# Performance work log

Hardware: AMD Instinct MI355X
Metric: run time of the kernel (lower is better)

## Reference

```python
import jax, jax.numpy as jnp
import numpy as np

N_MIN = 16
N_TABLES = 16
PER_LEVEL_SCALE = 1.3195079565048218
MAX_TABLE = 2 ** 19
H1, H2, H3 = 1, 2654435761, 805459861
OFFS = np.array([[0,0,0],[0,0,1],[0,1,0],[0,1,1],[1,0,0],[1,0,1],[1,1,0],[1,1,1]], dtype=np.int32)

def _levels():
    N_l, sizes, max_direct = [], [], 0
    for i in range(N_TABLES):
        res = int(np.ceil(N_MIN * np.exp(i * np.log(PER_LEVEL_SCALE)) - 1.0)) + 1
        ts = res ** 3
        ts = ts if ts % 8 == 0 else ((ts + 7) // 8) * 8
        ts = min(MAX_TABLE, ts)
        if ts == res ** 3:
            max_direct = i
        N_l.append(res); sizes.append(ts)
    return N_l, sizes, max_direct

N_L, SIZES, MAX_DIRECT = _levels()

def hash_encode(pos, grids):
    # pos: [N,3] in [0,1); grids: [16, MAX_TABLE, 2] (levels padded to MAX_TABLE)
    feats = []
    for l in range(N_TABLES):
        uvz = pos * jnp.float32(N_L[l])
        iuv_f = jnp.floor(uvz)
        f = uvz - iuv_f                                   # fractional part [N,3]
        corners = iuv_f.astype(jnp.int32)[:, None, :] + OFFS[None]  # [N,8,3]
        if l <= MAX_DIRECT:
            R = N_L[l]
            idx = (corners[..., 2] * (R * R) + corners[..., 1] * R + corners[..., 0]) % SIZES[l]
        else:
            cu = corners.astype(jnp.uint32)
            h = (cu[..., 0] * jnp.uint32(H1)) ^ (cu[..., 1] * jnp.uint32(H2)) ^ (cu[..., 2] * jnp.uint32(H3))
            idx = (h % jnp.uint32(SIZES[l])).astype(jnp.int32)
        c = grids[l][idx]                                 # gather -> [N,8,2]
        fx, fy, fz = f[:, 0:1], f[:, 1:2], f[:, 2:3]
        c00 = c[:, 0] * (1 - fx) + c[:, 4] * fx
        c01 = c[:, 1] * (1 - fx) + c[:, 5] * fx
        c10 = c[:, 2] * (1 - fx) + c[:, 6] * fx
        c11 = c[:, 3] * (1 - fx) + c[:, 7] * fx
        c0 = c00 * (1 - fy) + c10 * fy
        c1 = c01 * (1 - fy) + c11 * fy
        feats.append(c0 * (1 - fz) + c1 * fy)  # NOTE: c1*fy (not fz) replicates source exactly
    return jnp.concatenate(feats, axis=-1)  # [N, 32]

def setup_inputs():
    key = jax.random.key(0)
    ks = jax.random.split(key, 7)
    N = 1048576  # max_samples(512) * batch_size(2048)
    x = jax.random.uniform(ks[0], (N, 19), dtype=jnp.float32)  # pos(3) in [0,1) + dir feats(16)
    grids = (jax.random.uniform(ks[1], (N_TABLES, MAX_TABLE, 2), dtype=jnp.float32) * 2.0 - 1.0) * 1e-4
    h = 64
    w_sigma1 = jax.random.normal(ks[2], (32, h), dtype=jnp.float32) / np.sqrt(32).astype(np.float32)
    w_sigma2 = jax.random.normal(ks[3], (h, 16), dtype=jnp.float32) / np.sqrt(h).astype(np.float32)
    w_c1 = jax.random.normal(ks[4], (32, h), dtype=jnp.float32) / np.sqrt(32).astype(np.float32)
    w_c2 = jax.random.normal(ks[5], (h, h), dtype=jnp.float32) / np.sqrt(h).astype(np.float32)
    w_c3 = jax.random.normal(ks[6], (h, 3), dtype=jnp.float32) / np.sqrt(h).astype(np.float32)
    return {"x": x, "grids": grids, "w_sigma1": w_sigma1, "w_sigma2": w_sigma2,
            "w_c1": w_c1, "w_c2": w_c2, "w_c3": w_c3}

def reference(x, grids, w_sigma1, w_sigma2, w_c1, w_c2, w_c3):
    pos, direc = x[:, :3], x[:, 3:]
    enc = hash_encode(pos, grids)                       # [N,32]
    out = jax.nn.relu(enc @ w_sigma1) @ w_sigma2        # [N,16]
    sigma = out[:, 0]
    ci = jnp.concatenate([direc, out], axis=-1)         # [N,32]
    color = jax.nn.sigmoid(jax.nn.relu(jax.nn.relu(ci @ w_c1) @ w_c2) @ w_c3)  # [N,3]
    return jnp.concatenate([color, sigma[:, None]], axis=-1)  # [N,4]
```

## Files before the change

kernel.cpp:

```cpp
#include <hip/hip_runtime.h>
#include <math.h>


#define BLOCK 256
#define NTAB  (16*524288)
#define PITCH 88

constexpr int      kNL[16] = {16,22,28,37,49,65,85,112,148,195,257,338,446,589,777,1025};
constexpr unsigned kSZ[16] = {4096u,10648u,21952u,50656u,117656u,274632u,
                              524288u,524288u,524288u,524288u,524288u,
                              524288u,524288u,524288u,524288u,524288u};

typedef __attribute__((ext_vector_type(8))) short short8;
typedef __attribute__((ext_vector_type(4))) float float4v;

__device__ __forceinline__ short f2bf(float f) {
    unsigned u = __float_as_uint(f);
    unsigned r = u + 0x7fffu + ((u >> 16) & 1u);
    return (short)(r >> 16);
}
__device__ __forceinline__ float bf2f(short h) {
    return __uint_as_float(((unsigned)(unsigned short)h) << 16);
}
__device__ __forceinline__ unsigned pk2(float a, float b) {
    return ((unsigned)(unsigned short)f2bf(b) << 16) | (unsigned)(unsigned short)f2bf(a);
}
__device__ __forceinline__ float pe0(unsigned u) { return __uint_as_float(u << 16); }
__device__ __forceinline__ float pe1(unsigned u) { return __uint_as_float(u & 0xffff0000u); }

__device__ __forceinline__ unsigned trilerp_pack(const unsigned* vv, float fx, float fy, float fz)
{
    const float w0x = 1.f-fx, w0y = 1.f-fy, w0z = 1.f-fz;
    float e0, e1;
    {
        float c00 = pe0(vv[0])*w0x + pe0(vv[4])*fx;
        float c01 = pe0(vv[1])*w0x + pe0(vv[5])*fx;
        float c10 = pe0(vv[2])*w0x + pe0(vv[6])*fx;
        float c11 = pe0(vv[3])*w0x + pe0(vv[7])*fx;
        float c0 = c00*w0y + c10*fy;
        float c1 = c01*w0y + c11*fy;
        e0 = c0*w0z + c1*fy;
    }
    {
        float c00 = pe1(vv[0])*w0x + pe1(vv[4])*fx;
        float c01 = pe1(vv[1])*w0x + pe1(vv[5])*fx;
        float c10 = pe1(vv[2])*w0x + pe1(vv[6])*fx;
        float c11 = pe1(vv[3])*w0x + pe1(vv[7])*fx;
        float c0 = c00*w0y + c10*fy;
        float c1 = c01*w0y + c11*fy;
        e1 = c0*w0z + c1*fy;
    }
    return pk2(e0, e1);
}

__global__ void pack_pos(const float* __restrict__ x, float4* __restrict__ pos4, int n)
{
    int i = blockIdx.x * BLOCK + threadIdx.x;
    if (i >= n) return;
    const float* xr = x + (size_t)i * 19;
    pos4[i] = make_float4(xr[0], xr[1], xr[2], 0.f);
}

__global__ void conv_tables(const float* __restrict__ grids, unsigned* __restrict__ tbu)
{
    int i = blockIdx.x * BLOCK + threadIdx.x;
    if (i >= NTAB) return;
    float2 v = ((const float2*)grids)[i];
    tbu[i] = pk2(v.x, v.y);
}

__global__ void pack_wfrag(const float* __restrict__ w1, const float* __restrict__ w2,
                           const float* __restrict__ wc1, const float* __restrict__ wc2,
                           const float* __restrict__ wc3, uint4* __restrict__ wf)
{
    int lane = threadIdx.x;
    if (lane >= 64) return;
    int cn = lane & 15, q = lane >> 4;

    auto pack8 = [](const float* src, int stride) -> uint4 {
        uint4 r;
        r.x = pk2(src[0*stride], src[1*stride]);
        r.y = pk2(src[2*stride], src[3*stride]);
        r.z = pk2(src[4*stride], src[5*stride]);
        r.w = pk2(src[6*stride], src[7*stride]);
        return r;
    };

    int f = 0;
    for (int nt = 0; nt < 4; ++nt)
        wf[(f++)*64 + lane] = pack8(w1 + (q*8)*64 + nt*16 + cn, 64);
    for (int c = 0; c < 2; ++c)
        wf[(f++)*64 + lane] = pack8(w2 + (c*32 + q*8)*16 + cn, 16);
    for (int nt = 0; nt < 4; ++nt)
        wf[(f++)*64 + lane] = pack8(wc1 + (q*8)*64 + nt*16 + cn, 64);
    for (int c = 0; c < 2; ++c)
        for (int nt = 0; nt < 4; ++nt)
            wf[(f++)*64 + lane] = pack8(wc2 + (c*32 + q*8)*64 + nt*16 + cn, 64);
    for (int c = 0; c < 2; ++c) {
        if (cn < 3) wf[(f++)*64 + lane] = pack8(wc3 + (c*32 + q*8)*3 + cn, 3);
        else { uint4 z; z.x = z.y = z.z = z.w = 0u; wf[(f++)*64 + lane] = z; }
    }
}

template<int L>
__device__ __forceinline__ void gather4(const float4* __restrict__ pos4,
                                        const unsigned* __restrict__ tball,
                                        unsigned* __restrict__ encu,
                                        int n, int p0, int cnt)
{
    constexpr int R = kNL[L];
    constexpr unsigned S = kSZ[L];
    constexpr unsigned H2c = 2654435761u, H3c = 805459861u;
    const unsigned* __restrict__ tbu = tball + (size_t)L * 524288u;

    unsigned vv[4][8];
    float fxa[4], fya[4], fza[4];
    #pragma unroll
    for (int q = 0; q < 4; ++q) {
        if (q >= cnt) continue;
        float4 p = pos4[p0+q];
        const float Rf = (float)R;
        float ux = p.x*Rf, uy = p.y*Rf, uz = p.z*Rf;
        float gx = floorf(ux), gy = floorf(uy), gz = floorf(uz);
        fxa[q] = ux-gx; fya[q] = uy-gy; fza[q] = uz-gz;
        int ix = (int)gx, iy = (int)gy, iz = (int)gz;

        unsigned tc[4];
        #pragma unroll
        for (int c = 0; c < 4; ++c) {
            int yb = c >> 1, zb = c & 1;
            tc[c] = (unsigned)(iy+yb)*H2c ^ (unsigned)(iz+zb)*H3c;
        }
        if ((ix & 1) == 0) {
            #pragma unroll
            for (int c = 0; c < 4; ++c) {
                unsigned idx0 = ((unsigned)ix ^ tc[c]) & (S-1u);
                uint2 pr = *(const uint2*)(tbu + (idx0 & ~1u));
                unsigned swp = idx0 & 1u;
                vv[q][c]   = swp ? pr.y : pr.x;
                vv[q][4+c] = swp ? pr.x : pr.y;
            }
        } else {
            #pragma unroll
            for (int c = 0; c < 4; ++c) {
                unsigned idx0 = ((unsigned)ix     ^ tc[c]) & (S-1u);
                unsigned idx1 = ((unsigned)(ix+1) ^ tc[c]) & (S-1u);
                vv[q][c]   = tbu[idx0];
                vv[q][4+c] = tbu[idx1];
            }
        }
    }

    unsigned pkd[4];
    #pragma unroll
    for (int q = 0; q < 4; ++q) {
        if (q >= cnt) continue;
        pkd[q] = trilerp_pack(vv[q], fxa[q], fya[q], fza[q]);
    }

    unsigned* d = encu + (size_t)L*n + p0;
    if (cnt == 4) {
        uint4 o; o.x = pkd[0]; o.y = pkd[1]; o.z = pkd[2]; o.w = pkd[3];
        *(uint4*)d = o;
    } else {
        for (int q = 0; q < cnt; ++q) d[q] = pkd[q];
    }
}

__global__ __launch_bounds__(BLOCK)
void enc_all(const float4* __restrict__ pos4, const unsigned* __restrict__ tball,
             unsigned* __restrict__ encu, int n, int byA)
{
    const int bx = blockIdx.x;
    const int by = blockIdx.y;

    if (by < byA) {
        int p0 = (by*BLOCK + threadIdx.x) * 4;
        if (p0 >= n) return;
        int cnt = min(4, n - p0);
        switch (bx) {
            case 0: gather4< 6>(pos4,tball,encu,n,p0,cnt); break;
            case 1: gather4< 7>(pos4,tball,encu,n,p0,cnt); break;
            case 2: gather4< 8>(pos4,tball,encu,n,p0,cnt); break;
            case 3: gather4< 9>(pos4,tball,encu,n,p0,cnt); break;
            case 4: gather4<10>(pos4,tball,encu,n,p0,cnt); break;
            case 5: gather4<11>(pos4,tball,encu,n,p0,cnt); break;
            case 6: gather4<12>(pos4,tball,encu,n,p0,cnt); break;
            case 7: gather4<13>(pos4,tball,encu,n,p0,cnt); break;
        }
    } else {
        int q4 = (n + 3) / 4;
        int quarter = bx & 3;
        int jb = quarter * q4;
        int je = min(n, jb + q4);
        int p0 = jb + ((by-byA)*BLOCK + threadIdx.x) * 4;
        if (p0 >= je) return;
        int cnt = min(4, je - p0);
        if (bx < 4) gather4<14>(pos4,tball,encu,n,p0,cnt);
        else        gather4<15>(pos4,tball,encu,n,p0,cnt);
    }
}

template<int LV>
__device__ __forceinline__ void enc_addr(float4 p, const unsigned* __restrict__ tball,
                                         unsigned vv[8], float& fx, float& fy, float& fz)
{
    constexpr int R = kNL[LV];
    constexpr unsigned S = kSZ[LV];
    constexpr unsigned H2c = 2654435761u, H3c = 805459861u;
    const unsigned* __restrict__ tb = tball + (size_t)LV * 524288u;
    const float Rf = (float)R;
    float ux = p.x*Rf, uy = p.y*Rf, uz = p.z*Rf;
    float gx = floorf(ux), gy = floorf(uy), gz = floorf(uz);
    fx = ux-gx; fy = uy-gy; fz = uz-gz;
    int ix = (int)gx, iy = (int)gy, iz = (int)gz;

    if (LV >= 3) {
        unsigned tc[4];
        #pragma unroll
        for (int c = 0; c < 4; ++c) {
            int yb = c >> 1, zb = c & 1;
            tc[c] = (unsigned)(iy+yb)*H2c ^ (unsigned)(iz+zb)*H3c;
        }
        if ((ix & 1) == 0) {
            #pragma unroll
            for (int c = 0; c < 4; ++c) {
                unsigned h0 = (unsigned)ix ^ tc[c];
                unsigned base = (h0 & ~1u) % S;
                uint2 pr = *(const uint2*)(tb + base);
                unsigned swp = h0 & 1u;
                vv[c]   = swp ? pr.y : pr.x;
                vv[4+c] = swp ? pr.x : pr.y;
            }
        } else {
            #pragma unroll
            for (int c = 0; c < 4; ++c) {
                vv[c]   = tb[(((unsigned)ix)     ^ tc[c]) % S];
                vv[4+c] = tb[(((unsigned)(ix+1)) ^ tc[c]) % S];
            }
        }
    } else {
        #pragma unroll
        for (int j = 0; j < 8; ++j) {
            int ox = ix + ((j>>2)&1);
            int oy = iy + ((j>>1)&1);
            int oz = iz + (j&1);
            vv[j] = tb[(unsigned)((oz*(R*R) + oy*R + ox) % (int)S)];
        }
    }
}

__device__ __forceinline__ short8 ldfrag(const uint4* __restrict__ wf, int f, int lane) {
    union { uint4 u; short8 s; } cv;
    cv.u = wf[f*64 + lane];
    return cv.s;
}

__global__ __launch_bounds__(BLOCK)
void mlp_mfma(const float* __restrict__ x,
              const float4* __restrict__ pos4,
              const unsigned* __restrict__ tbu,
              const unsigned* __restrict__ encu,
              const uint4* __restrict__ wf,
              float* __restrict__ out, int n)
{
    __shared__ unsigned short s_scr[4][2][16*PITCH];
    __shared__ float s_sig[4][16];
    __shared__ float s_col[4][16][4];
    __shared__ float s_dir[4][304];
    __shared__ unsigned s_low[4][6][16];

    const int t = threadIdx.x;
    const int lane = t & 63;
    const int wave = t >> 6;
    const int m = lane & 15;
    const int q = lane >> 4;
    const int cn = m;
    const int blk = blockIdx.x * 64;
    const int pt  = blk + wave*16 + m;
    const int ptc = pt < n ? pt : n - 1;
    const int p0w = blk + wave*16;

    const float4v zero = {0.f, 0.f, 0.f, 0.f};

    {
        int npts = n - p0w; if (npts > 16) npts = 16; if (npts < 0) npts = 0;
        int nfl = npts * 19;
        const float* xs = x + (size_t)p0w * 19;
        float* sd = s_dir[wave];
        #pragma unroll
        for (int it = 0; it < 5; ++it) {
            int idx = it*64 + lane;
            if (idx < nfl) sd[idx] = xs[idx];
        }
    }

    {
        int lv = lane >> 4, pm = lane & 15;
        int pp = p0w + pm; if (pp >= n) pp = n - 1;
        float4 p = pos4[pp];
        unsigned vv[8]; float fx, fy, fz;
        switch (lv) {
            case 0: enc_addr<0>(p, tbu, vv, fx, fy, fz); break;
            case 1: enc_addr<1>(p, tbu, vv, fx, fy, fz); break;
            case 2: enc_addr<2>(p, tbu, vv, fx, fy, fz); break;
            default: enc_addr<3>(p, tbu, vv, fx, fy, fz); break;
        }
        s_low[wave][lv][pm] = trilerp_pack(vv, fx, fy, fz);
    }
    if (lane < 32) {
        int lv = 4 + (lane >> 4), pm = lane & 15;
        int pp = p0w + pm; if (pp >= n) pp = n - 1;
        float4 p = pos4[pp];
        unsigned vv[8]; float fx, fy, fz;
        if (lv == 4) enc_addr<4>(p, tbu, vv, fx, fy, fz);
        else         enc_addr<5>(p, tbu, vv, fx, fy, fz);
        s_low[wave][lv][pm] = trilerp_pack(vv, fx, fy, fz);
    }

    union { unsigned u[4]; short8 s; } a1;
    #pragma unroll
    for (int i = 0; i < 4; ++i) {
        int lv = q*4 + i;
        if (lv < 6) a1.u[i] = s_low[wave][lv][m];
        else        a1.u[i] = encu[(size_t)lv*n + ptc];
    }

    short8 bw1[4], bw2[2], bwc1[4];
    #pragma unroll
    for (int nt = 0; nt < 4; ++nt) bw1[nt] = ldfrag(wf, nt, lane);
    #pragma unroll
    for (int c = 0; c < 2; ++c)    bw2[c]  = ldfrag(wf, 4 + c, lane);
    #pragma unroll
    for (int nt = 0; nt < 4; ++nt) bwc1[nt] = ldfrag(wf, 6 + nt, lane);

    float4v h[4];
    #pragma unroll
    for (int nt = 0; nt < 4; ++nt) {
        h[nt] = __builtin_amdgcn_mfma_f32_16x16x32_bf16(a1.s, bw1[nt], zero, 0, 0, 0);
        #pragma unroll
        for (int r = 0; r < 4; ++r) h[nt][r] = fmaxf(h[nt][r], 0.f);
    }

    unsigned short* sA = &s_scr[wave][0][0];
    unsigned short* sB = &s_scr[wave][1][0];
    #pragma unroll
    for (int nt = 0; nt < 4; ++nt)
        #pragma unroll
        for (int r = 0; r < 4; ++r)
            sA[(q*4+r)*PITCH + nt*16 + cn] = (unsigned short)f2bf(h[nt][r]);
    short8 ah[2];
    #pragma unroll
    for (int c = 0; c < 2; ++c)
        ah[c] = *(const short8*)&sA[m*PITCH + c*32 + q*8];

    float4v o = __builtin_amdgcn_mfma_f32_16x16x32_bf16(ah[0], bw2[0], zero, 0, 0, 0);
    o = __builtin_amdgcn_mfma_f32_16x16x32_bf16(ah[1], bw2[1], o, 0, 0, 0);
    if (cn == 0) {
        #pragma unroll
        for (int r = 0; r < 4; ++r) s_sig[wave][q*4+r] = o[r];
    }

    #pragma unroll
    for (int r = 0; r < 4; ++r)
        sB[(q*4+r)*PITCH + cn] = (unsigned short)f2bf(o[r]);
    short8 ov = *(const short8*)&sB[m*PITCH + (q >= 2 ? (q-2)*8 : 0)];

    union { unsigned u[4]; short8 s; } ci_hi, ci_lo;
    if (q < 2) {
        const float* sd = s_dir[wave];
        int rm = ptc - p0w; if (rm < 0) rm = 0;
        #pragma unroll
        for (int i = 0; i < 4; ++i) {
            float d0 = sd[rm*19 + 3 + q*8 + 2*i];
            float d1 = sd[rm*19 + 3 + q*8 + 2*i + 1];
            short h0 = f2bf(d0), h1 = f2bf(d1);
            ci_hi.u[i] = ((unsigned)(unsigned short)h1 << 16) | (unsigned)(unsigned short)h0;
            short l0 = f2bf(d0 - bf2f(h0)), l1 = f2bf(d1 - bf2f(h1));
            ci_lo.u[i] = ((unsigned)(unsigned short)l1 << 16) | (unsigned)(unsigned short)l0;
        }
    } else {
        ci_hi.s = ov;
        #pragma unroll
        for (int i = 0; i < 4; ++i) ci_lo.u[i] = 0u;
    }

    float4v hc[4];
    #pragma unroll
    for (int nt = 0; nt < 4; ++nt) {
        hc[nt] = __builtin_amdgcn_mfma_f32_16x16x32_bf16(ci_hi.s, bwc1[nt], zero, 0, 0, 0);
        hc[nt] = __builtin_amdgcn_mfma_f32_16x16x32_bf16(ci_lo.s, bwc1[nt], hc[nt], 0, 0, 0);
        #pragma unroll
        for (int r = 0; r < 4; ++r) hc[nt][r] = fmaxf(hc[nt][r], 0.f);
    }

    short8 bwc2[2][4], bwc3[2];
    #pragma unroll
    for (int c = 0; c < 2; ++c)
        #pragma unroll
        for (int nt = 0; nt < 4; ++nt)
            bwc2[c][nt] = ldfrag(wf, 10 + c*4 + nt, lane);
    #pragma unroll
    for (int c = 0; c < 2; ++c) bwc3[c] = ldfrag(wf, 18 + c, lane);

    #pragma unroll
    for (int nt = 0; nt < 4; ++nt)
        #pragma unroll
        for (int r = 0; r < 4; ++r) {
            float v = hc[nt][r];
            short hi = f2bf(v);
            sA[(q*4+r)*PITCH + nt*16 + cn] = (unsigned short)hi;
            sB[(q*4+r)*PITCH + nt*16 + cn] = (unsigned short)f2bf(v - bf2f(hi));
        }
    short8 ghi[2], glo[2];
    #pragma unroll
    for (int c = 0; c < 2; ++c) {
        ghi[c] = *(const short8*)&sA[m*PITCH + c*32 + q*8];
        glo[c] = *(const short8*)&sB[m*PITCH + c*32 + q*8];
    }

    float4v g[4];
    #pragma unroll
    for (int nt = 0; nt < 4; ++nt) {
        float4v acc = __builtin_amdgcn_mfma_f32_16x16x32_bf16(ghi[0], bwc2[0][nt], zero, 0, 0, 0);
        acc = __builtin_amdgcn_mfma_f32_16x16x32_bf16(glo[0], bwc2[0][nt], acc, 0, 0, 0);
        acc = __builtin_amdgcn_mfma_f32_16x16x32_bf16(ghi[1], bwc2[1][nt], acc, 0, 0, 0);
        acc = __builtin_amdgcn_mfma_f32_16x16x32_bf16(glo[1], bwc2[1][nt], acc, 0, 0, 0);
        #pragma unroll
        for (int r = 0; r < 4; ++r) acc[r] = fmaxf(acc[r], 0.f);
        g[nt] = acc;
    }

    #pragma unroll
    for (int nt = 0; nt < 4; ++nt)
        #pragma unroll
        for (int r = 0; r < 4; ++r) {
            float v = g[nt][r];
            short hi = f2bf(v);
            sA[(q*4+r)*PITCH + nt*16 + cn] = (unsigned short)hi;
            sB[(q*4+r)*PITCH + nt*16 + cn] = (unsigned short)f2bf(v - bf2f(hi));
        }
    short8 uhi[2], ulo[2];
    #pragma unroll
    for (int c = 0; c < 2; ++c) {
        uhi[c] = *(const short8*)&sA[m*PITCH + c*32 + q*8];
        ulo[c] = *(const short8*)&sB[m*PITCH + c*32 + q*8];
    }

    float4v col = __builtin_amdgcn_mfma_f32_16x16x32_bf16(uhi[0], bwc3[0], zero, 0, 0, 0);
    col = __builtin_amdgcn_mfma_f32_16x16x32_bf16(ulo[0], bwc3[0], col, 0, 0, 0);
    col = __builtin_amdgcn_mfma_f32_16x16x32_bf16(uhi[1], bwc3[1], col, 0, 0, 0);
    col = __builtin_amdgcn_mfma_f32_16x16x32_bf16(ulo[1], bwc3[1], col, 0, 0, 0);
    #pragma unroll
    for (int r = 0; r < 4; ++r)
        col[r] = 1.f / (1.f + __expf(-col[r]));

    if (cn < 3) {
        #pragma unroll
        for (int r = 0; r < 4; ++r) s_col[wave][q*4+r][cn] = col[r];
    }

    __builtin_amdgcn_s_waitcnt(0);
    int pfi = lane >> 2, c4 = lane & 3;
    int pout = blk + wave*16 + pfi;
    if (pout < n) {
        float v = (c4 == 3) ? s_sig[wave][pfi] : s_col[wave][pfi][c4];
        out[(size_t)pout*4 + c4] = v;
    }
}

extern "C" void kernel_launch(void* const* d_in, const int* in_sizes, int n_in,
                              void* d_out, int out_size, void* d_ws, size_t ws_size,
                              hipStream_t stream) {
    const float* x     = (const float*)d_in[0];
    const float* grids = (const float*)d_in[1];
    const float* w1    = (const float*)d_in[2];
    const float* w2    = (const float*)d_in[3];
    const float* wc1   = (const float*)d_in[4];
    const float* wc2   = (const float*)d_in[5];
    const float* wc3   = (const float*)d_in[6];
    float* out = (float*)d_out;

    int n = in_sizes[0] / 19;
    size_t encB = (size_t)16 * n * sizeof(unsigned);
    size_t posB = (size_t)n * sizeof(float4);
    size_t tabB = (size_t)NTAB * sizeof(unsigned);

    char* p = (char*)d_ws;
    unsigned* encu = (unsigned*)p;
    float4*   pos4 = (float4*)(p + encB);
    unsigned* tbu  = (unsigned*)(p + encB + posB);
    uint4*    wf   = (uint4*)(p + encB + posB + tabB);

    pack_pos<<<(n + BLOCK - 1) / BLOCK, BLOCK, 0, stream>>>(x, pos4, n);
    conv_tables<<<(NTAB + BLOCK - 1) / BLOCK, BLOCK, 0, stream>>>(grids, tbu);
    pack_wfrag<<<1, 64, 0, stream>>>(w1, w2, wc1, wc2, wc3, wf);

    int byA = (n + BLOCK*4 - 1) / (BLOCK*4);
    int q4  = (n + 3) / 4;
    int byB = (q4 + BLOCK*4 - 1) / (BLOCK*4);
    dim3 ge(8, byA + byB);
    enc_all<<<ge, BLOCK, 0, stream>>>(pos4, tbu, encu, n, byA);

    mlp_mfma<<<(n + 63) / 64, BLOCK, 0, stream>>>(x, pos4, tbu, encu, wf, out, n);
}
```

Measured before the change: 554.3 us.

## Merge prep kernels into one launch and spread low-level encoding across waves

Combines the three preprocessing kernels (position packing, table bf16 conversion, weight fragment packing) into a single launch with block-range dispatch, removing two kernel launches and their gaps. In the MLP kernel, each wave now computes one low-resolution level for all 64 points of the block, so the level choice no longer diverges within a wave. The results are shared through block-level LDS, which requires a new __syncthreads. The encu loads for the high levels are hoisted to the top of the kernel so their latency overlaps with the low-level gathers.

```diff
diff --git a/kernel.cpp b/kernel.cpp
--- a/kernel.cpp
+++ b/kernel.cpp
@@ -53,52 +53,54 @@
     return pk2(e0, e1);
 }
 
-__global__ void pack_pos(const float* __restrict__ x, float4* __restrict__ pos4, int n)
+__global__ __launch_bounds__(BLOCK)
+void prep_all(const float* __restrict__ x, const float* __restrict__ grids,
+              const float* __restrict__ w1, const float* __restrict__ w2,
+              const float* __restrict__ wc1, const float* __restrict__ wc2,
+              const float* __restrict__ wc3,
+              float4* __restrict__ pos4, unsigned* __restrict__ tbu,
+              uint4* __restrict__ wf, int n, int nTabBlk, int nPosBlk)
 {
-    int i = blockIdx.x * BLOCK + threadIdx.x;
-    if (i >= n) return;
-    const float* xr = x + (size_t)i * 19;
-    pos4[i] = make_float4(xr[0], xr[1], xr[2], 0.f);
-}
-
-__global__ void conv_tables(const float* __restrict__ grids, unsigned* __restrict__ tbu)
-{
-    int i = blockIdx.x * BLOCK + threadIdx.x;
-    if (i >= NTAB) return;
-    float2 v = ((const float2*)grids)[i];
-    tbu[i] = pk2(v.x, v.y);
-}
-
-__global__ void pack_wfrag(const float* __restrict__ w1, const float* __restrict__ w2,
-                           const float* __restrict__ wc1, const float* __restrict__ wc2,
-                           const float* __restrict__ wc3, uint4* __restrict__ wf)
-{
-    int lane = threadIdx.x;
-    if (lane >= 64) return;
-    int cn = lane & 15, q = lane >> 4;
-
-    auto pack8 = [](const float* src, int stride) -> uint4 {
-        uint4 r;
-        r.x = pk2(src[0*stride], src[1*stride]);
-        r.y = pk2(src[2*stride], src[3*stride]);
-        r.z = pk2(src[4*stride], src[5*stride]);
-        r.w = pk2(src[6*stride], src[7*stride]);
-        return r;
-    };
-
-    int f = 0;
-    for (int nt = 0; nt < 4; ++nt)
-        wf[(f++)*64 + lane] = pack8(w1 + (q*8)*64 + nt*16 + cn, 64);
-    for (int c = 0; c < 2; ++c)
-        wf[(f++)*64 + lane] = pack8(w2 + (c*32 + q*8)*16 + cn, 16);
-    for (int nt = 0; nt < 4; ++nt)
-        wf[(f++)*64 + lane] = pack8(wc1 + (q*8)*64 + nt*16 + cn, 64);
-    for (int c = 0; c < 2; ++c)
-        for (int nt = 0; nt < 4; ++nt)
-            wf[(f++)*64 + lane] = pack8(wc2 + (c*32 + q*8)*64 + nt*16 + cn, 64);
-    for (int c = 0; c < 2; ++c) {
-        if (cn < 3) wf[(f++)*64 + lane] = pack8(wc3 + (c*32 + q*8)*3 + cn, 3);
-        else { uint4 z; z.x = z.y = z.z = z.w = 0u; wf[(f++)*64 + lane] = z; }
+    const int b = blockIdx.x;
+    if (b < nTabBlk) {
+        int i = b * BLOCK + threadIdx.x;
+        if (i < NTAB) {
+            float2 v = ((const float2*)grids)[i];
+            tbu[i] = pk2(v.x, v.y);
+        }
+    } else if (b < nTabBlk + nPosBlk) {
+        int i = (b - nTabBlk) * BLOCK + threadIdx.x;
+        if (i < n) {
+            const float* xr = x + (size_t)i * 19;
+            pos4[i] = make_float4(xr[0], xr[1], xr[2], 0.f);
+        }
+    } else {
+        int lane = threadIdx.x;
+        if (lane < 64) {
+            int cn = lane & 15, q = lane >> 4;
+            auto pack8 = [](const float* src, int stride) -> uint4 {
+                uint4 r;
+                r.x = pk2(src[0*stride], src[1*stride]);
+                r.y = pk2(src[2*stride], src[3*stride]);
+                r.z = pk2(src[4*stride], src[5*stride]);
+                r.w = pk2(src[6*stride], src[7*stride]);
+                return r;
+            };
+            int f = 0;
+            for (int nt = 0; nt < 4; ++nt)
+                wf[(f++)*64 + lane] = pack8(w1 + (q*8)*64 + nt*16 + cn, 64);
+            for (int c = 0; c < 2; ++c)
+                wf[(f++)*64 + lane] = pack8(w2 + (c*32 + q*8)*16 + cn, 16);
+            for (int nt = 0; nt < 4; ++nt)
+                wf[(f++)*64 + lane] = pack8(wc1 + (q*8)*64 + nt*16 + cn, 64);
+            for (int c = 0; c < 2; ++c)
+                for (int nt = 0; nt < 4; ++nt)
+                    wf[(f++)*64 + lane] = pack8(wc2 + (c*32 + q*8)*64 + nt*16 + cn, 64);
+            for (int c = 0; c < 2; ++c) {
+                if (cn < 3) wf[(f++)*64 + lane] = pack8(wc3 + (c*32 + q*8)*3 + cn, 3);
+                else { uint4 z; z.x = z.y = z.z = z.w = 0u; wf[(f++)*64 + lane] = z; }
+            }
+        }
     }
 }
 
@@ -108,9 +110,10 @@
                                         unsigned* __restrict__ encu,
                                         int n, int p0, int cnt)
 {
-    constexpr int R = kNL[L];
     constexpr unsigned S = kSZ[L];
     constexpr unsigned H2c = 2654435761u, H3c = 805459861u;
+    constexpr int R = kNL[L];
+    (void)R;
     const unsigned* __restrict__ tbu = tball + (size_t)L * 524288u;
 
     unsigned vv[4][8];
@@ -119,7 +122,7 @@
     for (int q = 0; q < 4; ++q) {
         if (q >= cnt) continue;
         float4 p = pos4[p0+q];
-        const float Rf = (float)R;
+        const float Rf = (float)kNL[L];
         float ux = p.x*Rf, uy = p.y*Rf, uz = p.z*Rf;
         float gx = floorf(ux), gy = floorf(uy), gz = floorf(uz);
         fxa[q] = ux-gx; fya[q] = uy-gy; fza[q] = uz-gz;
@@ -268,7 +271,7 @@
     __shared__ float s_sig[4][16];
     __shared__ float s_col[4][16][4];
     __shared__ float s_dir[4][304];
-    __shared__ unsigned s_low[4][6][16];
+    __shared__ unsigned s_lowB[6][64];
 
     const int t = threadIdx.x;
     const int lane = t & 63;
@@ -283,6 +286,13 @@
 
     const float4v zero = {0.f, 0.f, 0.f, 0.f};
 
+    unsigned encv[4];
+    #pragma unroll
+    for (int i = 0; i < 4; ++i) {
+        int lv = q*4 + i;
+        if (lv >= 6) encv[i] = encu[(size_t)lv*n + ptc];
+    }
+
     {
         int npts = n - p0w; if (npts > 16) npts = 16; if (npts < 0) npts = 0;
         int nfl = npts * 19;
@@ -296,34 +306,35 @@
     }
 
     {
-        int lv = lane >> 4, pm = lane & 15;
-        int pp = p0w + pm; if (pp >= n) pp = n - 1;
+        int pp = blk + lane; if (pp >= n) pp = n - 1;
         float4 p = pos4[pp];
         unsigned vv[8]; float fx, fy, fz;
-        switch (lv) {
-            case 0: enc_addr<0>(p, tbu, vv, fx, fy, fz); break;
-            case 1: enc_addr<1>(p, tbu, vv, fx, fy, fz); break;
-            case 2: enc_addr<2>(p, tbu, vv, fx, fy, fz); break;
+        switch (wave) {
+            case 0:  enc_addr<0>(p, tbu, vv, fx, fy, fz); break;
+            case 1:  enc_addr<1>(p, tbu, vv, fx, fy, fz); break;
+            case 2:  enc_addr<2>(p, tbu, vv, fx, fy, fz); break;
             default: enc_addr<3>(p, tbu, vv, fx, fy, fz); break;
         }
-        s_low[wave][lv][pm] = trilerp_pack(vv, fx, fy, fz);
+        s_lowB[wave][lane] = trilerp_pack(vv, fx, fy, fz);
     }
     if (lane < 32) {
-        int lv = 4 + (lane >> 4), pm = lane & 15;
-        int pp = p0w + pm; if (pp >= n) pp = n - 1;
+        int lv = 4 + (wave >> 1);
+        int pb2 = (wave & 1)*32 + lane;
+        int pp = blk + pb2; if (pp >= n) pp = n - 1;
         float4 p = pos4[pp];
         unsigned vv[8]; float fx, fy, fz;
         if (lv == 4) enc_addr<4>(p, tbu, vv, fx, fy, fz);
         else         enc_addr<5>(p, tbu, vv, fx, fy, fz);
-        s_low[wave][lv][pm] = trilerp_pack(vv, fx, fy, fz);
-    }
+        s_lowB[lv][pb2] = trilerp_pack(vv, fx, fy, fz);
+    }
+    __syncthreads();
 
     union { unsigned u[4]; short8 s; } a1;
     #pragma unroll
     for (int i = 0; i < 4; ++i) {
         int lv = q*4 + i;
-        if (lv < 6) a1.u[i] = s_low[wave][lv][m];
-        else        a1.u[i] = encu[(size_t)lv*n + ptc];
+        if (lv < 6) a1.u[i] = s_lowB[lv][wave*16 + m];
+        else        a1.u[i] = encv[i];
     }
 
     short8 bw1[4], bw2[2], bwc1[4];
@@ -492,9 +503,10 @@
     unsigned* tbu  = (unsigned*)(p + encB + posB);
     uint4*    wf   = (uint4*)(p + encB + posB + tabB);
 
-    pack_pos<<<(n + BLOCK - 1) / BLOCK, BLOCK, 0, stream>>>(x, pos4, n);
-    conv_tables<<<(NTAB + BLOCK - 1) / BLOCK, BLOCK, 0, stream>>>(grids, tbu);
-    pack_wfrag<<<1, 64, 0, stream>>>(w1, w2, wc1, wc2, wc3, wf);
+    int nTabBlk = (NTAB + BLOCK - 1) / BLOCK;
+    int nPosBlk = (n + BLOCK - 1) / BLOCK;
+    prep_all<<<nTabBlk + nPosBlk + 1, BLOCK, 0, stream>>>(
+        x, grids, w1, w2, wc1, wc2, wc3, pos4, tbu, wf, n, nTabBlk, nPosBlk);
 
     int byA = (n + BLOCK*4 - 1) / (BLOCK*4);
     int q4  = (n + 3) / 4;
```

Result: faster. 532.4 us (-4.0%).
